# Performance work log

Hardware: AMD Instinct MI355X
Metric: run time of the kernel (lower is better)

## Reference

```python
import jax, jax.numpy as jnp
import numpy as np

B = 256            # batch_size
N_IN = 4096        # kernel^2 * in_n_capsules (kernel=1 for FC)
N_OUT = 32         # out_n_capsules
POSE_DIM = 16      # in_d_capsules
MPD = 4            # matrix_pose_dim = sqrt(POSE_DIM)


def setup_inputs() -> dict:
    key = jax.random.key(0)
    k1, k2, k3 = jax.random.split(key, 3)
    current_pose = jax.random.normal(k1, (B, N_IN, POSE_DIM), dtype=jnp.float32)
    # nn.Parameter(0.02 * randn(kernel, kernel, in_n, mpd, mpd)) with kernel=1
    w_current = 0.02 * jax.random.normal(k2, (1, 1, N_IN, MPD, MPD), dtype=jnp.float32)
    # nn.Parameter(0.02 * randn(out_n, mpd, mpd))
    w_next = 0.02 * jax.random.normal(k3, (N_OUT, MPD, MPD), dtype=jnp.float32)
    return {"current_pose": current_pose, "w_current": w_current, "w_next": w_next,
            "h_out": 1, "w_out": 1}


def reference(current_pose, w_current, w_next, h_out, w_out):
    # FC layer: h_out = w_out = 1, kernel_size = 1
    b = current_pose.shape[0]
    n_in = w_current.shape[0] * w_current.shape[1] * w_current.shape[2]
    mpd = w_current.shape[-1]
    pose_dim = mpd * mpd
    n_out = w_next.shape[0]

    wc = w_current.reshape(n_in, mpd, mpd)[None]        # (1, n_in, mpd, mpd)
    wn = w_next[None]                                    # (1, n_out, mpd, mpd)

    # pose transform by w_current: (b, n_in, mpd, mpd) @ (1, n_in, mpd, mpd)
    cp = current_pose.reshape(b, n_in, mpd, mpd)
    cp = jnp.matmul(cp, wc).reshape(b, n_in, pose_dim)   # (b, n_in, pose_dim)

    # dots: constant pose_dim**-0.5, softmax over out-capsule axis (dim=-2)
    scale = pose_dim ** (-0.5)
    dots = jax.nn.softmax(jnp.full((b, n_out, n_in), scale, dtype=cp.dtype), axis=-2)

    # route: (b, n_out, n_in) x (b, n_in, pose_dim) -> (b, n_out, pose_dim)
    npc = jnp.einsum('bij,bje->bie', dots, cp)

    # pose transform by w_next
    npc = npc.reshape(b, n_out, mpd, mpd)
    npc = jnp.matmul(npc, wn)

    return npc.reshape(b, 1, 1, n_out, pose_dim)
```

## Files before the change

### kernel.cpp

```cpp
#include <hip/hip_runtime.h>


#define BATCH 256
#define NIN   4096
#define NOUT  32

constexpr int THREADS = 512;
constexpr int JPT     = NIN / THREADS;
constexpr int WAVES   = THREADS / 64;

typedef __attribute__((ext_vector_type(4))) float f32x4;

__global__ __launch_bounds__(THREADS)
void caps_fused(const float* __restrict__ cp,
                const float* __restrict__ wc,
                const float* __restrict__ wn,
                float* __restrict__ out) {
    const int b    = blockIdx.x;
    const int t    = threadIdx.x;
    const int lane = t & 63;
    const int wave = t >> 6;

    float acc[16];
#pragma unroll
    for (int e = 0; e < 16; ++e) acc[e] = 0.f;

    const f32x4* cp4 = (const f32x4*)(cp + ((size_t)b * NIN + t) * 16);
    const f32x4* wc4 = (const f32x4*)(wc + (size_t)t * 16);
    constexpr int STRIDE = THREADS * 4;

#pragma unroll
    for (int it = 0; it < JPT; ++it) {
        f32x4 a[4], w[4];
#pragma unroll
        for (int v = 0; v < 4; ++v) {
            a[v] = cp4[it * STRIDE + v];
            w[v] = wc4[it * STRIDE + v];
        }
#pragma unroll
        for (int r = 0; r < 4; ++r)
#pragma unroll
            for (int c = 0; c < 4; ++c)
#pragma unroll
                for (int k = 0; k < 4; ++k)
                    acc[r * 4 + c] += a[r][k] * w[k][c];
    }

    {
        const bool hi1 = lane & 1;
#pragma unroll
        for (int e = 0; e < 8; ++e) {
            float a0 = acc[e], a1 = acc[e + 8];
            float send = hi1 ? a0 : a1;
            float keep = hi1 ? a1 : a0;
            acc[e] = keep + __shfl_xor(send, 1);
        }
        const bool hi2 = lane & 2;
#pragma unroll
        for (int e = 0; e < 4; ++e) {
            float a0 = acc[e], a1 = acc[e + 4];
            float send = hi2 ? a0 : a1;
            float keep = hi2 ? a1 : a0;
            acc[e] = keep + __shfl_xor(send, 2);
        }
        const bool hi4 = lane & 4;
#pragma unroll
        for (int e = 0; e < 2; ++e) {
            float a0 = acc[e], a1 = acc[e + 2];
            float send = hi4 ? a0 : a1;
            float keep = hi4 ? a1 : a0;
            acc[e] = keep + __shfl_xor(send, 4);
        }
        {
            const bool hi8 = lane & 8;
            float a0 = acc[0], a1 = acc[1];
            float send = hi8 ? a0 : a1;
            float keep = hi8 ? a1 : a0;
            acc[0] = keep + __shfl_xor(send, 8);
        }
        acc[0] += __shfl_xor(acc[0], 16);
        acc[0] += __shfl_xor(acc[0], 32);
    }

    __shared__ float red[WAVES][16];
    __shared__ float S[16];
    if (lane < 16) {
        const int e = ((lane & 1) ? 8 : 0) | ((lane & 2) ? 4 : 0) |
                      ((lane & 4) ? 2 : 0) | ((lane & 8) ? 1 : 0);
        red[wave][e] = acc[0];
    }
    __syncthreads();

    if (t < 16) {
        float v = 0.f;
#pragma unroll
        for (int w2 = 0; w2 < WAVES; ++w2) v += red[w2][t];
        S[t] = v * (1.0f / 32.0f);
    }
    __syncthreads();

    if (t < NOUT * 4) {
        const int i = t >> 2;
        const int r = t & 3;
        const f32x4* wn4 = (const f32x4*)(wn + i * 16);
        f32x4 w0 = wn4[0], w1 = wn4[1], w2 = wn4[2], w3 = wn4[3];
        float s0 = S[r * 4 + 0], s1 = S[r * 4 + 1], s2 = S[r * 4 + 2], s3 = S[r * 4 + 3];
        f32x4 o;
        o[0] = s0 * w0[0] + s1 * w1[0] + s2 * w2[0] + s3 * w3[0];
        o[1] = s0 * w0[1] + s1 * w1[1] + s2 * w2[1] + s3 * w3[1];
        o[2] = s0 * w0[2] + s1 * w1[2] + s2 * w2[2] + s3 * w3[2];
        o[3] = s0 * w0[3] + s1 * w1[3] + s2 * w2[3] + s3 * w3[3];
        ((f32x4*)(out + (size_t)b * NOUT * 16))[t] = o;
    }
}

extern "C" void kernel_launch(void* const* d_in, const int* in_sizes, int n_in,
                              void* d_out, int out_size, void* d_ws, size_t ws_size,
                              hipStream_t stream) {
    const float* cp = (const float*)d_in[0];
    const float* wc = (const float*)d_in[1];
    const float* wn = (const float*)d_in[2];
    float* out = (float*)d_out;

    caps_fused<<<BATCH, THREADS, 0, stream>>>(cp, wc, wn, out);
}
```

Measured before the change: 19.49 us.

## Assign one pose row per thread with coalesced loads and quad swizzle broadcast

Each thread now handles one 4-float row of a 4x4 pose matrix instead of a whole matrix. Loads become fully contiguous, lane-strided f32x4 accesses, and the weight columns are shared across the quad with ds_swizzle broadcasts. Block size doubles to 1024 threads and the cross-lane reduction shrinks to four accumulators. This is meant to improve memory coalescing and cut register pressure, at the cost of extra swizzle instructions and a larger block.

```diff
diff --git a/kernel.cpp b/kernel.cpp
--- a/kernel.cpp
+++ b/kernel.cpp
@@ -5,11 +5,24 @@
 #define NIN   4096
 #define NOUT  32
 
-constexpr int THREADS = 512;
-constexpr int JPT     = NIN / THREADS;
+constexpr int THREADS = 1024;
+constexpr int VPT     = 4;
+constexpr int POS     = NIN * 4;
+constexpr int ITERS   = POS / (THREADS * VPT);
 constexpr int WAVES   = THREADS / 64;
 
 typedef __attribute__((ext_vector_type(4))) float f32x4;
+
+template<int K>
+__device__ __forceinline__ f32x4 quad_bcast(f32x4 x) {
+    constexpr int imm = 0x8000 | (0x55 * K);
+    f32x4 r;
+#pragma unroll
+    for (int d = 0; d < 4; ++d)
+        r[d] = __int_as_float(
+            __builtin_amdgcn_ds_swizzle(__float_as_int(x[d]), imm));
+    return r;
+}
 
 __global__ __launch_bounds__(THREADS)
 void caps_fused(const float* __restrict__ cp,
@@ -21,80 +34,49 @@
     const int lane = t & 63;
     const int wave = t >> 6;
 
-    float acc[16];
-#pragma unroll
-    for (int e = 0; e < 16; ++e) acc[e] = 0.f;
+    const f32x4* cp4 = (const f32x4*)cp + (size_t)b * POS;
+    const f32x4* wc4 = (const f32x4*)wc;
 
-    const f32x4* cp4 = (const f32x4*)(cp + ((size_t)b * NIN + t) * 16);
-    const f32x4* wc4 = (const f32x4*)(wc + (size_t)t * 16);
-    constexpr int STRIDE = THREADS * 4;
+    f32x4 acc = {0.f, 0.f, 0.f, 0.f};
 
 #pragma unroll
-    for (int it = 0; it < JPT; ++it) {
-        f32x4 a[4], w[4];
+    for (int it = 0; it < ITERS; ++it) {
+        f32x4 a[VPT], w[VPT];
 #pragma unroll
-        for (int v = 0; v < 4; ++v) {
-            a[v] = cp4[it * STRIDE + v];
-            w[v] = wc4[it * STRIDE + v];
+        for (int v = 0; v < VPT; ++v) {
+            const int p = it * (THREADS * VPT) + v * THREADS + t;
+            a[v] = cp4[p];
+            w[v] = wc4[p];
         }
 #pragma unroll
-        for (int r = 0; r < 4; ++r)
-#pragma unroll
-            for (int c = 0; c < 4; ++c)
-#pragma unroll
-                for (int k = 0; k < 4; ++k)
-                    acc[r * 4 + c] += a[r][k] * w[k][c];
+        for (int v = 0; v < VPT; ++v) {
+            const f32x4 w0 = quad_bcast<0>(w[v]);
+            const f32x4 w1 = quad_bcast<1>(w[v]);
+            const f32x4 w2 = quad_bcast<2>(w[v]);
+            const f32x4 w3 = quad_bcast<3>(w[v]);
+            acc += a[v][0] * w0;
+            acc += a[v][1] * w1;
+            acc += a[v][2] * w2;
+            acc += a[v][3] * w3;
+        }
     }
 
-    {
-        const bool hi1 = lane & 1;
 #pragma unroll
-        for (int e = 0; e < 8; ++e) {
-            float a0 = acc[e], a1 = acc[e + 8];
-            float send = hi1 ? a0 : a1;
-            float keep = hi1 ? a1 : a0;
-            acc[e] = keep + __shfl_xor(send, 1);
-        }
-        const bool hi2 = lane & 2;
+    for (int m = 4; m <= 32; m <<= 1) {
 #pragma unroll
-        for (int e = 0; e < 4; ++e) {
-            float a0 = acc[e], a1 = acc[e + 4];
-            float send = hi2 ? a0 : a1;
-            float keep = hi2 ? a1 : a0;
-            acc[e] = keep + __shfl_xor(send, 2);
-        }
-        const bool hi4 = lane & 4;
-#pragma unroll
-        for (int e = 0; e < 2; ++e) {
-            float a0 = acc[e], a1 = acc[e + 2];
-            float send = hi4 ? a0 : a1;
-            float keep = hi4 ? a1 : a0;
-            acc[e] = keep + __shfl_xor(send, 4);
-        }
-        {
-            const bool hi8 = lane & 8;
-            float a0 = acc[0], a1 = acc[1];
-            float send = hi8 ? a0 : a1;
-            float keep = hi8 ? a1 : a0;
-            acc[0] = keep + __shfl_xor(send, 8);
-        }
-        acc[0] += __shfl_xor(acc[0], 16);
-        acc[0] += __shfl_xor(acc[0], 32);
+        for (int c = 0; c < 4; ++c)
+            acc[c] += __shfl_xor(acc[c], m, 64);
     }
 
-    __shared__ float red[WAVES][16];
+    __shared__ f32x4 red[WAVES][4];
     __shared__ float S[16];
-    if (lane < 16) {
-        const int e = ((lane & 1) ? 8 : 0) | ((lane & 2) ? 4 : 0) |
-                      ((lane & 4) ? 2 : 0) | ((lane & 8) ? 1 : 0);
-        red[wave][e] = acc[0];
-    }
+    if (lane < 4) red[wave][lane] = acc;
     __syncthreads();
 
     if (t < 16) {
         float v = 0.f;
 #pragma unroll
-        for (int w2 = 0; w2 < WAVES; ++w2) v += red[w2][t];
+        for (int w2 = 0; w2 < WAVES; ++w2) v += red[w2][t >> 2][t & 3];
         S[t] = v * (1.0f / 32.0f);
     }
     __syncthreads();
@@ -103,8 +85,9 @@
         const int i = t >> 2;
         const int r = t & 3;
         const f32x4* wn4 = (const f32x4*)(wn + i * 16);
-        f32x4 w0 = wn4[0], w1 = wn4[1], w2 = wn4[2], w3 = wn4[3];
-        float s0 = S[r * 4 + 0], s1 = S[r * 4 + 1], s2 = S[r * 4 + 2], s3 = S[r * 4 + 3];
+        const f32x4 w0 = wn4[0], w1 = wn4[1], w2 = wn4[2], w3 = wn4[3];
+        const float s0 = S[r * 4 + 0], s1 = S[r * 4 + 1];
+        const float s2 = S[r * 4 + 2], s3 = S[r * 4 + 3];
         f32x4 o;
         o[0] = s0 * w0[0] + s1 * w1[0] + s2 * w2[0] + s3 * w3[0];
         o[1] = s0 * w0[1] + s1 * w1[1] + s2 * w2[1] + s3 * w3[1];
```

Result: faster. 17.78 us (-8.8%).
